# Optimization experiments

Measured on AMD Instinct MI355X. Metric: run time of the kernel, lower is better.

## Reference

```python
import jax, jax.numpy as jnp
import numpy as np

D = 1280
RANK = 4

def _lora(x, down, up):
    # x: [..., in]; down: [r, in]; up: [out, r]
    return (x @ down.T) @ up.T

def setup_inputs() -> dict:
    key = jax.random.key(0)
    ks = jax.random.split(key, 15)
    B, S = 4, 2048
    inp = {
        'hidden_states': jax.random.normal(ks[0], (B, S, D), jnp.float32),
        'Wq': jax.random.normal(ks[1], (D, D), jnp.float32) * (D ** -0.5),
        'Wk': jax.random.normal(ks[2], (D, D), jnp.float32) * (D ** -0.5),
        'Wv': jax.random.normal(ks[3], (D, D), jnp.float32) * (D ** -0.5),
        'Wo': jax.random.normal(ks[4], (D, D), jnp.float32) * (D ** -0.5),
        'bo': jax.random.normal(ks[5], (D,), jnp.float32) * 0.02,
        'q_down': jax.random.normal(ks[6], (RANK, D), jnp.float32) / RANK,
        'q_up': jax.random.normal(ks[7], (D, RANK), jnp.float32) * 0.02,
        'k_down': jax.random.normal(ks[8], (RANK, D), jnp.float32) / RANK,
        'k_up': jax.random.normal(ks[9], (D, RANK), jnp.float32) * 0.02,
        'v_down': jax.random.normal(ks[10], (RANK, D), jnp.float32) / RANK,
        'v_up': jax.random.normal(ks[11], (D, RANK), jnp.float32) * 0.02,
        'o_down': jax.random.normal(ks[12], (RANK, D), jnp.float32) / RANK,
        'o_up': jax.random.normal(ks[13], (D, RANK), jnp.float32) * 0.02,
        'num_heads': 8,
    }
    return inp

def reference(hidden_states, Wq, Wk, Wv, Wo, bo, q_down, q_up, k_down, k_up,
              v_down, v_up, o_down, o_up, num_heads):
    B, S, Dm = hidden_states.shape
    H = num_heads
    hd = Dm // H
    scale = hd ** -0.5
    x = hidden_states
    # base projections + rank-4 LoRA deltas (self-attention: enc == x)
    q = x @ Wq.T + _lora(x, q_down, q_up)
    k = x @ Wk.T + _lora(x, k_down, k_up)
    v = x @ Wv.T + _lora(x, v_down, v_up)
    q = q.reshape(B, S, H, hd)
    k = k.reshape(B, S, H, hd)
    v = v.reshape(B, S, H, hd)
    # explicit bmm -> softmax -> bmm attention (no mask, no norm_cross)
    scores = jnp.einsum('bqhd,bkhd->bhqk', q, k) * scale  # [B,H,S,S]
    probs = jax.nn.softmax(scores, axis=-1)
    ctx = jnp.einsum('bhqk,bkhd->bqhd', probs, v).reshape(B, S, Dm)
    # output projection (with bias) + LoRA on output; dropout is identity at eval
    out = ctx @ Wo.T + bo + _lora(ctx, o_down, o_up)
    return out
```

## Files before the change

### kernel.cpp

```cpp
#include <hip/hip_runtime.h>
#include <cstdint>

typedef _Float16 f16;
typedef f16 f16x8 __attribute__((ext_vector_type(8)));
typedef f16 f16x4 __attribute__((ext_vector_type(4)));
typedef f16 f16x2 __attribute__((ext_vector_type(2)));
typedef float f32x4 __attribute__((ext_vector_type(4)));
typedef uint32_t u32x4 __attribute__((ext_vector_type(4)));

#define D_MODEL 1280
#define SEQ 2048
#define BATCH 4
#define HEADS 8
#define HDIM 160
#define MTOT (BATCH*SEQ)
#define NQKV (3*D_MODEL)

__device__ __forceinline__ void gload_lds16(const f16* g, f16* l) {
  __builtin_amdgcn_global_load_lds(
      (const __attribute__((address_space(1))) unsigned int*)g,
      (__attribute__((address_space(3))) unsigned int*)l,
      16, 0, 0);
}

#define BARX() { asm volatile("" ::: "memory"); __builtin_amdgcn_s_barrier(); asm volatile("" ::: "memory"); }
#define VMW(N) { asm volatile("s_waitcnt vmcnt(" #N ")" ::: "memory"); }


__global__ void convert_f32_to_f16(const float* __restrict__ in, f16* __restrict__ out, int n4) {
  int i = blockIdx.x * 256 + threadIdx.x;
  if (i < n4) {
    float4 v = ((const float4*)in)[i];
    f16x4 o = { (f16)v.x, (f16)v.y, (f16)v.z, (f16)v.w };
    ((f16x4*)out)[i] = o;
  }
}

__global__ void build_weff4(const float* __restrict__ W0, const float* __restrict__ W1,
                            const float* __restrict__ W2, const float* __restrict__ W3,
                            const float* __restrict__ u0, const float* __restrict__ u1,
                            const float* __restrict__ u2, const float* __restrict__ u3,
                            const float* __restrict__ n0, const float* __restrict__ n1,
                            const float* __restrict__ n2, const float* __restrict__ n3,
                            f16* __restrict__ o0, f16* __restrict__ o1,
                            f16* __restrict__ o2, f16* __restrict__ o3) {
  int which = blockIdx.y;
  const float* W    = which==0 ? W0 : which==1 ? W1 : which==2 ? W2 : W3;
  const float* up   = which==0 ? u0 : which==1 ? u1 : which==2 ? u2 : u3;
  const float* down = which==0 ? n0 : which==1 ? n1 : which==2 ? n2 : n3;
  f16* out          = which==0 ? o0 : which==1 ? o1 : which==2 ? o2 : o3;
  int idx = blockIdx.x * 256 + threadIdx.x;
  int o  = idx / (D_MODEL / 4);
  int i0 = (idx % (D_MODEL / 4)) * 4;
  float4 w = *(const float4*)&W[(size_t)o * D_MODEL + i0];
  float p0 = up[o*4+0], p1 = up[o*4+1], p2 = up[o*4+2], p3 = up[o*4+3];
  float vals[4] = { w.x, w.y, w.z, w.w };
  f16x4 r;
#pragma unroll
  for (int j = 0; j < 4; ++j) {
    int i = i0 + j;
    float acc = vals[j] + p0*down[i] + p1*down[D_MODEL + i]
                        + p2*down[2*D_MODEL + i] + p3*down[3*D_MODEL + i];
    r[j] = (f16)acc;
  }
  *(f16x4*)&out[(size_t)o * D_MODEL + i0] = r;
}

__global__ void transpose_v(const f16* __restrict__ qkv, f16* __restrict__ Vt) {
  __shared__ f16 t[32][36];
  int s0 = blockIdx.x * 32;
  int d0 = blockIdx.y * 32;
  int bh = blockIdx.z;
  int b = bh >> 3, h = bh & 7;
  int tid = threadIdx.x;
  {
    int i = tid >> 3, j4 = (tid & 7) * 4;
    *(f16x4*)&t[i][j4] =
        *(const f16x4*)&qkv[(size_t)(b*SEQ + s0 + i) * NQKV + 2*D_MODEL + h*HDIM + d0 + j4];
  }
  __syncthreads();
  {
    int dd = tid >> 3, s4 = (tid & 7) * 4;
    f16x4 v;
#pragma unroll
    for (int k = 0; k < 4; ++k) {
      int s = s4 + k;
      int sj = (((s>>2) ^ (s>>3)) & 1) ? (s ^ 12) : s;
      v[k] = t[sj][dd];
    }
    *(f16x4*)&Vt[(size_t)(bh*HDIM + d0 + dd) * SEQ + s0 + s4] = v;
  }
}

template<int OUTF32>
__global__ __launch_bounds__(512) void gemm256(const f16* __restrict__ A,
                                               const f16* __restrict__ Bw,
                                               void* __restrict__ Cp, int ldc,
                                               const float* __restrict__ bias) {
  const int K = D_MODEL, NT = D_MODEL/64;
  __shared__ alignas(16) f16 lds[7 * 8192];
  f16* LB = lds + 3*8192;
  int tid = threadIdx.x;
  int wv = tid >> 6, l = tid & 63;
  int wm = wv >> 2, wn = wv & 3;
  int lr = l & 15, lg = l >> 4;

  int flat = blockIdx.y * gridDim.x + blockIdx.x;
  int bnn = gridDim.x;
  int xcd = flat & 7, idx = flat >> 3;
  int bm = xcd * 4 + idx / bnn;
  int bn = idx % bnn;

  int row0 = tid >> 3;
  int csw  = ((tid & 7) ^ (row0 & 7)) * 8;
  const f16* Asrc[2]; const f16* Bsrc[2];
#pragma unroll
  for (int h = 0; h < 2; ++h) {
    Asrc[h] = A  + (size_t)(bm*256 + h*128 + row0) * K + csw;
    Bsrc[h] = Bw + (size_t)(bn*256 + h*128 + row0) * K + csw;
  }
  int ldsoff = wv * 512;

  int xsl0 = ((lg)     ^ (lr & 7)) * 8;
  int xsl1 = ((4 + lg) ^ (lr & 7)) * 8;

  f32x4 acc[8][4] = {};

#define STAGE_A(h, slot, kt) { const f16* s_ = Asrc[h] + (kt)*64; f16* d_ = lds + (slot)*8192 + ldsoff; \
    gload_lds16(s_, d_); gload_lds16(s_ + (size_t)64*K, d_ + 4096); }
#define STAGE_B(h, slot, kt) { const f16* s_ = Bsrc[h] + (kt)*64; f16* d_ = LB + (slot)*8192 + ldsoff; \
    gload_lds16(s_, d_); gload_lds16(s_ + (size_t)64*K, d_ + 4096); }

  STAGE_A(0, 0, 0); STAGE_A(1, 1, 0);
  STAGE_B(0, 0, 0); STAGE_B(1, 1, 0);
  STAGE_B(0, 2, 1);
  VMW(2); BARX();

  for (int t = 0; t < NT; ++t) {
    int sA0 = (2*t) % 3, sA1 = (2*t+1) % 3, sA2 = (2*t+2) % 3;
    int sB0 = (2*t) & 3, sB1 = (2*t+1) & 3, sB3 = (2*t+3) & 3;
    int tc1 = (t+1 < NT) ? t+1 : NT-1;
    int tc2 = (t+2 < NT) ? t+2 : NT-1;

#define PHASE(ah, bh, sA, sB, STG, VMOPT) { \
    f16x8 af[4][2], bf[2][2]; \
    _Pragma("unroll") \
    for (int j = 0; j < 4; ++j) { \
      int base = (sA)*8192 + (wm*64 + j*16 + lr)*64; \
      af[j][0] = *(const f16x8*)&lds[base + xsl0]; \
      af[j][1] = *(const f16x8*)&lds[base + xsl1]; \
    } \
    _Pragma("unroll") \
    for (int i = 0; i < 2; ++i) { \
      int base = (sB)*8192 + (wn*32 + i*16 + lr)*64; \
      bf[i][0] = *(const f16x8*)&LB[base + xsl0]; \
      bf[i][1] = *(const f16x8*)&LB[base + xsl1]; \
    } \
    STG; \
    BARX(); \
    __builtin_amdgcn_s_setprio(1); \
    _Pragma("unroll") \
    for (int j = 0; j < 4; ++j) \
      _Pragma("unroll") \
      for (int i = 0; i < 2; ++i) { \
        acc[(ah)*4+j][(bh)*2+i] = __builtin_amdgcn_mfma_f32_16x16x32_f16(af[j][0], bf[i][0], acc[(ah)*4+j][(bh)*2+i], 0, 0, 0); \
        acc[(ah)*4+j][(bh)*2+i] = __builtin_amdgcn_mfma_f32_16x16x32_f16(af[j][1], bf[i][1], acc[(ah)*4+j][(bh)*2+i], 0, 0, 0); \
      } \
    __builtin_amdgcn_s_setprio(0); \
    VMOPT; \
    BARX(); }

    PHASE(0, 0, sA0, sB0, STAGE_B(1, sB3, tc1), VMW(2))
    PHASE(1, 0, sA1, sB0, STAGE_A(0, sA2, tc1), )
    PHASE(0, 1, sA0, sB1, STAGE_B(0, sB0, tc2), )
    PHASE(1, 1, sA1, sB1, STAGE_A(1, sA0, tc1), VMW(4))
#undef PHASE
  }

#pragma unroll
  for (int mf = 0; mf < 8; ++mf) {
    int r0 = bm*256 + (mf>>2)*128 + wm*64 + (mf&3)*16 + lg*4;
#pragma unroll
    for (int nf = 0; nf < 4; ++nf) {
      int c = bn*256 + (nf>>1)*128 + wn*32 + (nf&1)*16 + lr;
      if constexpr (OUTF32) {
        float bb = bias[c];
#pragma unroll
        for (int rg = 0; rg < 4; ++rg)
          ((float*)Cp)[(size_t)(r0 + rg) * ldc + c] = acc[mf][nf][rg] + bb;
      } else {
#pragma unroll
        for (int rg = 0; rg < 4; ++rg)
          ((f16*)Cp)[(size_t)(r0 + rg) * ldc + c] = (f16)acc[mf][nf][rg];
      }
    }
  }
#undef STAGE_A
#undef STAGE_B
}

__global__ __launch_bounds__(256, 2) void attn(const f16* __restrict__ qkv,
                                               const f16* __restrict__ Vt,
                                               f16* __restrict__ ctx) {
  __shared__ alignas(16) f16 Kl[64 * 168];
  __shared__ alignas(16) f16 Vl[160 * 64];
  int tid = threadIdx.x;
  int wv = tid >> 6, l = tid & 63;
  int lr = l & 15, lg = l >> 4;
  int flat = blockIdx.y * 16 + blockIdx.x;
  int xcd = flat & 7, idx = flat >> 3;
  int bh = xcd * 4 + (idx >> 4);
  int qt = idx & 15;
  int b = bh >> 3, h = bh & 7;
  size_t qrow[2];
#pragma unroll
  for (int qg = 0; qg < 2; ++qg)
    qrow[qg] = (size_t)(b*SEQ + qt*128 + wv*32 + qg*16 + lr);

  const f16 qscale = (f16)0.114055069f;
  f16x8 qf[2][5];
#pragma unroll
  for (int qg = 0; qg < 2; ++qg)
#pragma unroll
    for (int dk = 0; dk < 5; ++dk) {
      f16x8 t = *(const f16x8*)&qkv[qrow[qg] * NQKV + h*HDIM + dk*32 + lg*8];
#pragma unroll
      for (int j = 0; j < 8; ++j) t[j] = t[j] * qscale;
      qf[qg][dk] = t;
    }

  const char* Kg0 = (const char*)qkv + (size_t)(b*SEQ)*NQKV*2 + (size_t)D_MODEL*2 + (size_t)h*HDIM*2;
  char* KlB = (char*)Kl;
  uint32_t koff[6];
  f16* kld[6];
#pragma unroll
  for (int it = 0; it < 6; ++it) {
    int p = (it < 5) ? it*256 + tid : 1280 + (tid & 63);
    koff[it] = (uint32_t)(p/21) * (NQKV*2) + (uint32_t)(p%21) * 16;
    kld[it] = (f16*)(KlB + ((it < 5) ? (it*256 + wv*64)*16 : 1280*16));
  }

  const char* Vg0 = (const char*)Vt + (size_t)bh*HDIM*SEQ*2;
  char* VlB = (char*)Vl;
  uint32_t voff[5];
  f16* vld[5];
#pragma unroll
  for (int it = 0; it < 5; ++it) {
    int c = it*256 + tid;
    int row = c >> 3, sp = c & 7;
    voff[it] = (uint32_t)row * (SEQ*2) + (uint32_t)((sp ^ (row & 7)) * 16);
    vld[it] = (f16*)(VlB + (it*256 + wv*64)*16);
  }
  uint32_t vro[2];
#pragma unroll
  for (int ks = 0; ks < 2; ++ks)
    vro[ks] = (uint32_t)lr*128 + (uint32_t)((((ks*4+lg) ^ (lr & 7)) * 16));

  f32x4 oacc[10][2] = {};
  float m[2] = {-1e30f, -1e30f}, lsum[2] = {0.f, 0.f};

  for (int kt = 0; kt < 32; ++kt) {
    const char* Ksrc = Kg0 + (size_t)kt * (64*NQKV*2);
    const char* Vsrc = Vg0 + (size_t)kt * 128;
#pragma unroll
    for (int it = 0; it < 5; ++it) {
      gload_lds16((const f16*)(Ksrc + koff[it]), kld[it]);
      gload_lds16((const f16*)(Vsrc + voff[it]), vld[it]);
    }
    if (wv == 0)
      gload_lds16((const f16*)(Ksrc + koff[5]), kld[5]);
    __syncthreads();

    f32x4 sc[4][2] = {};
    __builtin_amdgcn_s_setprio(1);
#pragma unroll
    for (int kb = 0; kb < 4; ++kb)
#pragma unroll
      for (int dk = 0; dk < 5; ++dk) {
        f16x8 a = *(const f16x8*)&Kl[(kb*16 + lr)*168 + dk*32 + lg*8];
        sc[kb][0] = __builtin_amdgcn_mfma_f32_16x16x32_f16(a, qf[0][dk], sc[kb][0], 0, 0, 0);
        sc[kb][1] = __builtin_amdgcn_mfma_f32_16x16x32_f16(a, qf[1][dk], sc[kb][1], 0, 0, 0);
      }
    __builtin_amdgcn_s_setprio(0);

    float smax[2];
#pragma unroll
    for (int qg = 0; qg < 2; ++qg) {
      float a0 = fmaxf(fmaxf(sc[0][qg][0], sc[0][qg][1]), fmaxf(sc[0][qg][2], sc[0][qg][3]));
      float a1 = fmaxf(fmaxf(sc[1][qg][0], sc[1][qg][1]), fmaxf(sc[1][qg][2], sc[1][qg][3]));
      float a2 = fmaxf(fmaxf(sc[2][qg][0], sc[2][qg][1]), fmaxf(sc[2][qg][2], sc[2][qg][3]));
      float a3 = fmaxf(fmaxf(sc[3][qg][0], sc[3][qg][1]), fmaxf(sc[3][qg][2], sc[3][qg][3]));
      float sm = fmaxf(fmaxf(a0, a1), fmaxf(a2, a3));
      sm = fmaxf(sm, __shfl_xor(sm, 16));
      sm = fmaxf(sm, __shfl_xor(sm, 32));
      smax[qg] = sm;
    }
    if (!__all(fmaxf(smax[0] - m[0], smax[1] - m[1]) <= 11.54f)) {
#pragma unroll
      for (int qg = 0; qg < 2; ++qg) {
        float mn = fmaxf(m[qg], smax[qg]);
        float alpha = exp2f(m[qg] - mn);
#pragma unroll
        for (int df = 0; df < 10; ++df)
#pragma unroll
          for (int rg = 0; rg < 4; ++rg) oacc[df][qg][rg] *= alpha;
        lsum[qg] *= alpha;
        m[qg] = mn;
      }
    }

    f16x8 pb[2][2];
#pragma unroll
    for (int qg = 0; qg < 2; ++qg) {
      float ps[16];
#pragma unroll
      for (int kb = 0; kb < 4; ++kb)
#pragma unroll
        for (int rg = 0; rg < 4; ++rg)
          ps[kb*4 + rg] = exp2f(sc[kb][qg][rg] - m[qg]);
      float s0 = (ps[0] + ps[1]) + (ps[2] + ps[3]);
      float s1 = (ps[4] + ps[5]) + (ps[6] + ps[7]);
      float s2 = (ps[8] + ps[9]) + (ps[10] + ps[11]);
      float s3 = (ps[12] + ps[13]) + (ps[14] + ps[15]);
      lsum[qg] += (s0 + s1) + (s2 + s3);

      uint32_t w0, w1, w2, w3, w4, w5, w6, w7;
      asm("v_cvt_pkrtz_f16_f32 %0, %1, %2" : "=v"(w0) : "v"(ps[0]),  "v"(ps[1]));
      asm("v_cvt_pkrtz_f16_f32 %0, %1, %2" : "=v"(w1) : "v"(ps[2]),  "v"(ps[3]));
      asm("v_cvt_pkrtz_f16_f32 %0, %1, %2" : "=v"(w2) : "v"(ps[4]),  "v"(ps[5]));
      asm("v_cvt_pkrtz_f16_f32 %0, %1, %2" : "=v"(w3) : "v"(ps[6]),  "v"(ps[7]));
      asm("v_cvt_pkrtz_f16_f32 %0, %1, %2" : "=v"(w4) : "v"(ps[8]),  "v"(ps[9]));
      asm("v_cvt_pkrtz_f16_f32 %0, %1, %2" : "=v"(w5) : "v"(ps[10]), "v"(ps[11]));
      asm("v_cvt_pkrtz_f16_f32 %0, %1, %2" : "=v"(w6) : "v"(ps[12]), "v"(ps[13]));
      asm("v_cvt_pkrtz_f16_f32 %0, %1, %2" : "=v"(w7) : "v"(ps[14]), "v"(ps[15]));
      asm("v_permlane32_swap_b32 %0, %1" : "+v"(w0), "+v"(w2));
      asm("v_permlane32_swap_b32 %0, %1" : "+v"(w1), "+v"(w3));
      asm("v_permlane32_swap_b32 %0, %1" : "+v"(w4), "+v"(w6));
      asm("v_permlane32_swap_b32 %0, %1" : "+v"(w5), "+v"(w7));
      u32x4 c0 = { w0, w1, w2, w3 };
      u32x4 c1 = { w4, w5, w6, w7 };
      pb[qg][0] = __builtin_bit_cast(f16x8, c0);
      pb[qg][1] = __builtin_bit_cast(f16x8, c1);
    }

    __builtin_amdgcn_s_setprio(1);
#pragma unroll
    for (int df = 0; df < 10; ++df)
#pragma unroll
      for (int ks = 0; ks < 2; ++ks) {
        f16x8 a = *(const f16x8*)(VlB + vro[ks] + df*2048);
        oacc[df][0] = __builtin_amdgcn_mfma_f32_16x16x32_f16(a, pb[0][ks], oacc[df][0], 0, 0, 0);
        oacc[df][1] = __builtin_amdgcn_mfma_f32_16x16x32_f16(a, pb[1][ks], oacc[df][1], 0, 0, 0);
      }
    __builtin_amdgcn_s_setprio(0);
    __syncthreads();
  }

#pragma unroll
  for (int qg = 0; qg < 2; ++qg) {
    lsum[qg] += __shfl_xor(lsum[qg], 16);
    lsum[qg] += __shfl_xor(lsum[qg], 32);
  }

#pragma unroll
  for (int qg = 0; qg < 2; ++qg) {
    float inv = 1.f / lsum[qg];
#pragma unroll
    for (int df = 0; df < 10; ++df)
#pragma unroll
      for (int pr = 0; pr < 2; ++pr) {
        f16x2 pv = { (f16)(oacc[df][qg][pr*2+0] * inv), (f16)(oacc[df][qg][pr*2+1] * inv) };
        *(f16x2*)&ctx[qrow[qg] * D_MODEL + h*HDIM + df*16 + lg*4 + pr*2] = pv;
      }
  }
}


extern "C" void kernel_launch(void* const* d_in, const int* in_sizes, int n_in,
                              void* d_out, int out_size, void* d_ws, size_t ws_size,
                              hipStream_t stream) {
  const float* x   = (const float*)d_in[0];
  const float* Wq  = (const float*)d_in[1];
  const float* Wk  = (const float*)d_in[2];
  const float* Wv  = (const float*)d_in[3];
  const float* Wo  = (const float*)d_in[4];
  const float* bo  = (const float*)d_in[5];
  const float* q_down = (const float*)d_in[6];
  const float* q_up   = (const float*)d_in[7];
  const float* k_down = (const float*)d_in[8];
  const float* k_up   = (const float*)d_in[9];
  const float* v_down = (const float*)d_in[10];
  const float* v_up   = (const float*)d_in[11];
  const float* o_down = (const float*)d_in[12];
  const float* o_up   = (const float*)d_in[13];
  float* out = (float*)d_out;

  char* ws = (char*)d_ws;
  f16* xh    = (f16*)ws;
  f16* Wqkv  = (f16*)(ws + 20971520);
  f16* WoE   = (f16*)(ws + 20971520 + 9830400);
  f16* qkv   = (f16*)(ws + 20971520 + 9830400 + 3276800);
  f16* Vt    = (f16*)(ws + 20971520 + 9830400 + 3276800 + 62914560);
  f16* ctx   = xh;

  convert_f32_to_f16<<<(MTOT*D_MODEL/4 + 255)/256, 256, 0, stream>>>(x, xh, MTOT*D_MODEL/4);
  build_weff4<<<dim3(D_MODEL*D_MODEL/4/256, 4), 256, 0, stream>>>(
      Wq, Wk, Wv, Wo, q_up, k_up, v_up, o_up, q_down, k_down, v_down, o_down,
      Wqkv, Wqkv + (size_t)D_MODEL*D_MODEL, Wqkv + (size_t)2*D_MODEL*D_MODEL, WoE);

  gemm256<0><<<dim3(NQKV/256, MTOT/256), 512, 0, stream>>>(xh, Wqkv, qkv, NQKV, nullptr);
  transpose_v<<<dim3(SEQ/32, HDIM/32, BATCH*HEADS), 256, 0, stream>>>(qkv, Vt);
  attn<<<dim3(SEQ/128, BATCH*HEADS), 256, 0, stream>>>(qkv, Vt, ctx);
  gemm256<1><<<dim3(D_MODEL/256, MTOT/256), 512, 0, stream>>>(ctx, WoE, out, D_MODEL, bo);
  (void)in_sizes; (void)n_in; (void)out_size; (void)ws_size;
}
```

Measured before the change: 272.6 us.

## Fuse V transpose into QKV GEMM epilogue and merge prep kernels

Merges the f32-to-f16 conversion and the effective-weight builder into one launch, and drops the separate V transpose kernel. The QKV GEMM now writes V tiles straight into the transposed, swizzled Vt layout from its epilogue. This removes two kernel launches and one read and write of the V slice of qkv. In exchange the V epilogue uses scattered 8-byte stores strided by SEQ, which may coalesce poorly.

```diff
diff --git a/kernel.cpp b/kernel.cpp
--- a/kernel.cpp
+++ b/kernel.cpp
@@ -26,35 +26,35 @@
 #define BARX() { asm volatile("" ::: "memory"); __builtin_amdgcn_s_barrier(); asm volatile("" ::: "memory"); }
 #define VMW(N) { asm volatile("s_waitcnt vmcnt(" #N ")" ::: "memory"); }
 
-
-__global__ void convert_f32_to_f16(const float* __restrict__ in, f16* __restrict__ out, int n4) {
-  int i = blockIdx.x * 256 + threadIdx.x;
-  if (i < n4) {
-    float4 v = ((const float4*)in)[i];
+__global__ void prep(const float* __restrict__ x, f16* __restrict__ xh,
+                     const float* __restrict__ W0, const float* __restrict__ W1,
+                     const float* __restrict__ W2, const float* __restrict__ W3,
+                     const float* __restrict__ u0, const float* __restrict__ u1,
+                     const float* __restrict__ u2, const float* __restrict__ u3,
+                     const float* __restrict__ n0, const float* __restrict__ n1,
+                     const float* __restrict__ n2, const float* __restrict__ n3,
+                     f16* __restrict__ o0, f16* __restrict__ o1,
+                     f16* __restrict__ o2, f16* __restrict__ o3) {
+  int bid = blockIdx.x;
+  if (bid < 10240) {
+    int i = bid * 256 + threadIdx.x;
+    float4 v = ((const float4*)x)[i];
     f16x4 o = { (f16)v.x, (f16)v.y, (f16)v.z, (f16)v.w };
-    ((f16x4*)out)[i] = o;
-  }
-}
-
-__global__ void build_weff4(const float* __restrict__ W0, const float* __restrict__ W1,
-                            const float* __restrict__ W2, const float* __restrict__ W3,
-                            const float* __restrict__ u0, const float* __restrict__ u1,
-                            const float* __restrict__ u2, const float* __restrict__ u3,
-                            const float* __restrict__ n0, const float* __restrict__ n1,
-                            const float* __restrict__ n2, const float* __restrict__ n3,
-                            f16* __restrict__ o0, f16* __restrict__ o1,
-                            f16* __restrict__ o2, f16* __restrict__ o3) {
-  int which = blockIdx.y;
+    ((f16x4*)xh)[i] = o;
+    return;
+  }
+  int w = bid - 10240;
+  int which = w / 1600;
   const float* W    = which==0 ? W0 : which==1 ? W1 : which==2 ? W2 : W3;
   const float* up   = which==0 ? u0 : which==1 ? u1 : which==2 ? u2 : u3;
   const float* down = which==0 ? n0 : which==1 ? n1 : which==2 ? n2 : n3;
   f16* out          = which==0 ? o0 : which==1 ? o1 : which==2 ? o2 : o3;
-  int idx = blockIdx.x * 256 + threadIdx.x;
+  int idx = (w % 1600) * 256 + threadIdx.x;
   int o  = idx / (D_MODEL / 4);
   int i0 = (idx % (D_MODEL / 4)) * 4;
-  float4 w = *(const float4*)&W[(size_t)o * D_MODEL + i0];
+  float4 wv = *(const float4*)&W[(size_t)o * D_MODEL + i0];
   float p0 = up[o*4+0], p1 = up[o*4+1], p2 = up[o*4+2], p3 = up[o*4+3];
-  float vals[4] = { w.x, w.y, w.z, w.w };
+  float vals[4] = { wv.x, wv.y, wv.z, wv.w };
   f16x4 r;
 #pragma unroll
   for (int j = 0; j < 4; ++j) {
@@ -66,37 +66,12 @@
   *(f16x4*)&out[(size_t)o * D_MODEL + i0] = r;
 }
 
-__global__ void transpose_v(const f16* __restrict__ qkv, f16* __restrict__ Vt) {
-  __shared__ f16 t[32][36];
-  int s0 = blockIdx.x * 32;
-  int d0 = blockIdx.y * 32;
-  int bh = blockIdx.z;
-  int b = bh >> 3, h = bh & 7;
-  int tid = threadIdx.x;
-  {
-    int i = tid >> 3, j4 = (tid & 7) * 4;
-    *(f16x4*)&t[i][j4] =
-        *(const f16x4*)&qkv[(size_t)(b*SEQ + s0 + i) * NQKV + 2*D_MODEL + h*HDIM + d0 + j4];
-  }
-  __syncthreads();
-  {
-    int dd = tid >> 3, s4 = (tid & 7) * 4;
-    f16x4 v;
-#pragma unroll
-    for (int k = 0; k < 4; ++k) {
-      int s = s4 + k;
-      int sj = (((s>>2) ^ (s>>3)) & 1) ? (s ^ 12) : s;
-      v[k] = t[sj][dd];
-    }
-    *(f16x4*)&Vt[(size_t)(bh*HDIM + d0 + dd) * SEQ + s0 + s4] = v;
-  }
-}
-
-template<int OUTF32>
+template<int OUTMODE>
 __global__ __launch_bounds__(512) void gemm256(const f16* __restrict__ A,
                                                const f16* __restrict__ Bw,
                                                void* __restrict__ Cp, int ldc,
-                                               const float* __restrict__ bias) {
+                                               const float* __restrict__ bias,
+                                               f16* __restrict__ Vt) {
   const int K = D_MODEL, NT = D_MODEL/64;
   __shared__ alignas(16) f16 lds[7 * 8192];
   f16* LB = lds + 3*8192;
@@ -177,21 +152,40 @@
 #undef PHASE
   }
 
-#pragma unroll
-  for (int mf = 0; mf < 8; ++mf) {
-    int r0 = bm*256 + (mf>>2)*128 + wm*64 + (mf&3)*16 + lg*4;
+  if (OUTMODE == 2 && bn >= 10) {
 #pragma unroll
     for (int nf = 0; nf < 4; ++nf) {
-      int c = bn*256 + (nf>>1)*128 + wn*32 + (nf&1)*16 + lr;
-      if constexpr (OUTF32) {
-        float bb = bias[c];
-#pragma unroll
-        for (int rg = 0; rg < 4; ++rg)
-          ((float*)Cp)[(size_t)(r0 + rg) * ldc + c] = acc[mf][nf][rg] + bb;
-      } else {
-#pragma unroll
-        for (int rg = 0; rg < 4; ++rg)
-          ((f16*)Cp)[(size_t)(r0 + rg) * ldc + c] = (f16)acc[mf][nf][rg];
+      int c  = bn*256 + (nf>>1)*128 + wn*32 + (nf&1)*16 + lr;
+      int cv = c - 2*D_MODEL;
+      int hh = cv / HDIM, d = cv % HDIM;
+#pragma unroll
+      for (int mf = 0; mf < 8; ++mf) {
+        int r0 = bm*256 + (mf>>2)*128 + wm*64 + (mf&3)*16 + lg*4;
+        int b = r0 >> 11, s0 = r0 & (SEQ-1);
+        int soff = s0 & 31, sblk = s0 & ~31;
+        int sj = (((soff>>2) ^ (soff>>3)) & 1) ? (soff ^ 12) : soff;
+        f16x4 v = { (f16)acc[mf][nf][0], (f16)acc[mf][nf][1],
+                    (f16)acc[mf][nf][2], (f16)acc[mf][nf][3] };
+        *(f16x4*)&Vt[(size_t)((b*HEADS + hh)*HDIM + d) * SEQ + sblk + sj] = v;
+      }
+    }
+  } else {
+#pragma unroll
+    for (int mf = 0; mf < 8; ++mf) {
+      int r0 = bm*256 + (mf>>2)*128 + wm*64 + (mf&3)*16 + lg*4;
+#pragma unroll
+      for (int nf = 0; nf < 4; ++nf) {
+        int c = bn*256 + (nf>>1)*128 + wn*32 + (nf&1)*16 + lr;
+        if constexpr (OUTMODE == 1) {
+          float bb = bias[c];
+#pragma unroll
+          for (int rg = 0; rg < 4; ++rg)
+            ((float*)Cp)[(size_t)(r0 + rg) * ldc + c] = acc[mf][nf][rg] + bb;
+        } else {
+#pragma unroll
+          for (int rg = 0; rg < 4; ++rg)
+            ((f16*)Cp)[(size_t)(r0 + rg) * ldc + c] = (f16)acc[mf][nf][rg];
+        }
       }
     }
   }
@@ -403,14 +397,12 @@
   f16* Vt    = (f16*)(ws + 20971520 + 9830400 + 3276800 + 62914560);
   f16* ctx   = xh;
 
-  convert_f32_to_f16<<<(MTOT*D_MODEL/4 + 255)/256, 256, 0, stream>>>(x, xh, MTOT*D_MODEL/4);
-  build_weff4<<<dim3(D_MODEL*D_MODEL/4/256, 4), 256, 0, stream>>>(
+  prep<<<16640, 256, 0, stream>>>(x, xh,
       Wq, Wk, Wv, Wo, q_up, k_up, v_up, o_up, q_down, k_down, v_down, o_down,
       Wqkv, Wqkv + (size_t)D_MODEL*D_MODEL, Wqkv + (size_t)2*D_MODEL*D_MODEL, WoE);
 
-  gemm256<0><<<dim3(NQKV/256, MTOT/256), 512, 0, stream>>>(xh, Wqkv, qkv, NQKV, nullptr);
-  transpose_v<<<dim3(SEQ/32, HDIM/32, BATCH*HEADS), 256, 0, stream>>>(qkv, Vt);
+  gemm256<2><<<dim3(NQKV/256, MTOT/256), 512, 0, stream>>>(xh, Wqkv, qkv, NQKV, nullptr, Vt);
   attn<<<dim3(SEQ/128, BATCH*HEADS), 256, 0, stream>>>(qkv, Vt, ctx);
-  gemm256<1><<<dim3(D_MODEL/256, MTOT/256), 512, 0, stream>>>(ctx, WoE, out, D_MODEL, bo);
+  gemm256<1><<<dim3(D_MODEL/256, MTOT/256), 512, 0, stream>>>(ctx, WoE, out, D_MODEL, bo, nullptr);
   (void)in_sizes; (void)n_in; (void)out_size; (void)ws_size;
 }
```

Result: no change. 267.5 us (-1.9%).
